# Kernel optimization log

Measured on AMD Instinct MI355X. Metric: run time of the kernel, lower is better.

Reference implementation:

```python
import jax, jax.numpy as jnp
import numpy as np

B, N, E = 2, 2048, 1024
H, D = 16, 64  # num_heads, head_dim
BASE = 10000.0
EPS = 1e-5


def _lrpe(x, offset=0):
    """xmixers Lrpe (lrpe_type=1): activation (silu) then rotary position embedding.
    x: [b, n, h, d] -> [b, n, h, d]"""
    x = jax.nn.silu(x)
    b, n, h, d = x.shape
    inv_freq = BASE ** (-(jnp.arange(d // 2, dtype=jnp.float32) * 2.0) / d)  # [d/2]
    pos = jnp.arange(n, dtype=jnp.float32) + offset
    ang = pos[:, None] * inv_freq[None, :]            # [n, d/2]
    cos = jnp.cos(ang)[None, :, None, :].astype(x.dtype)
    sin = jnp.sin(ang)[None, :, None, :].astype(x.dtype)
    x1, x2 = x[..., : d // 2], x[..., d // 2:]
    return jnp.concatenate([x1 * cos - x2 * sin, x1 * sin + x2 * cos], axis=-1)


def setup_inputs() -> dict:
    key = jax.random.key(0)
    ks = jax.random.split(key, 8)
    std = 0.02
    return {
        "x": jax.random.normal(ks[0], (B, N, E), dtype=jnp.float32),
        "Wq": jax.random.normal(ks[1], (E, E), dtype=jnp.float32) * std,
        "Wk": jax.random.normal(ks[2], (E, E), dtype=jnp.float32) * std,
        "Wv": jax.random.normal(ks[3], (E, E), dtype=jnp.float32) * std,
        "Wo": jax.random.normal(ks[4], (E, E), dtype=jnp.float32) * std,
        "Wg1": jax.random.normal(ks[5], (E, D), dtype=jnp.float32) * std,
        "Wg2": jax.random.normal(ks[6], (D, E), dtype=jnp.float32) * std,
        "gamma": jnp.ones((E,), dtype=jnp.float32),
        "beta": jnp.zeros((E,), dtype=jnp.float32),
    }


def reference(x, Wq, Wk, Wv, Wo, Wg1, Wg2, gamma, beta):
    b, n, e = x.shape
    q = (x @ Wq).reshape(b, n, H, D)
    k = (x @ Wk).reshape(b, n, H, D)
    v = (x @ Wv).reshape(b, n, H, D)

    q = _lrpe(q, offset=0)
    k = _lrpe(k, offset=0)

    # causal linear attention: (q k^T * tril) @ v, no softmax
    energy = jnp.einsum('bnhd,bmhd->bhnm', q, k)            # [b,h,n,n]
    mask = jnp.tril(jnp.ones((n, n), dtype=x.dtype))
    energy = energy * mask
    out = jnp.einsum('bhnm,bmhd->bnhd', energy, v).reshape(b, n, e)

    # output gate: sigmoid(Linear(Linear(x)))
    gate = jax.nn.sigmoid((x @ Wg1) @ Wg2)
    out = out * gate

    # layernorm over embed_dim
    mu = jnp.mean(out, axis=-1, keepdims=True)
    var = jnp.mean(jnp.square(out - mu), axis=-1, keepdims=True)
    out = (out - mu) * jax.lax.rsqrt(var + EPS) * gamma + beta

    return out @ Wo
```

## Files before the change

kernel.cpp:

```cpp
#include <hip/hip_runtime.h>
#include <hip/hip_bf16.h>
#include <math.h>

#define B_ 2
#define N_ 2048
#define E_ 1024
#define H_ 16
#define D_ 64
#define HALF_ 32
#define CK 64
#define NC (N_/CK)
#define BN (B_*N_)
#define TLD 72
#define EPS_ 1e-5f
#define NQKV 3200

using bf16x8  = __attribute__((ext_vector_type(8))) short;
using f32x4   = __attribute__((ext_vector_type(4))) float;
using short4v = __attribute__((ext_vector_type(4))) short;

__device__ __forceinline__ float sigmoid_(float v){ return 1.0f/(1.0f + __expf(-v)); }

__device__ __forceinline__ unsigned short f2bf(float f){
  unsigned u = __float_as_uint(f);
  unsigned r = (u + 0x7fffu + ((u>>16)&1u)) >> 16;
  return (unsigned short)r;
}
__device__ __forceinline__ float bf2f(unsigned short h){
  return __uint_as_float(((unsigned)h)<<16);
}

#define GLDS16(gp, lp) __builtin_amdgcn_global_load_lds( \
    (const __attribute__((address_space(1))) void*)(gp), \
    (__attribute__((address_space(3))) void*)(lp), 16, 0, 0)

__global__ __launch_bounds__(256) void sincos_kernel(float* __restrict__ ct,
                                                     float* __restrict__ st){
  int i = blockIdx.x*256 + threadIdx.x;
  int n = i >> 5, j = i & (HALF_-1);
  double invf = exp(((double)(-2*j)/(double)D_) * log(10000.0));
  double ang = (double)n * invf;
  ct[i] = (float)cos(ang);
  st[i] = (float)sin(ang);
}

__global__ __launch_bounds__(256) void xsplit_kernel(const float* __restrict__ x,
    short* __restrict__ xh, short* __restrict__ xl){
  int i = blockIdx.x*256 + threadIdx.x;
  float4 vv = ((const float4*)x)[i];
  float vs[4] = {vv.x, vv.y, vv.z, vv.w};
  short4v h, l;
  #pragma unroll
  for (int j=0;j<4;j++){
    unsigned short hb = f2bf(vs[j]);
    h[j] = (short)hb;
    l[j] = (short)f2bf(vs[j] - bf2f(hb));
  }
  ((short4v*)xh)[i] = h;
  ((short4v*)xl)[i] = l;
}

__global__ __launch_bounds__(256) void zfill_kernel(short* __restrict__ a,
                                                    short* __restrict__ b){
  int i = blockIdx.x*256 + threadIdx.x;
  short4v z = {0,0,0,0};
  ((short4v*)a)[i] = z;
  ((short4v*)b)[i] = z;
}

__global__ __launch_bounds__(256) void wsplit_kernel(const float* __restrict__ W,
    short* __restrict__ Wth, short* __restrict__ Wtl, int K, int N){
  __shared__ float T[64][65];
  int k0 = blockIdx.x*64, n0 = blockIdx.y*64;
  int tid = threadIdx.x;
  #pragma unroll
  for (int it=0; it<4; ++it){
    int idx = it*256 + tid;
    int r = idx >> 4, c = (idx & 15) << 2;
    float4 v = *(const float4*)&W[(size_t)(k0+r)*N + n0 + c];
    T[c+0][r]=v.x; T[c+1][r]=v.y; T[c+2][r]=v.z; T[c+3][r]=v.w;
  }
  __syncthreads();
  #pragma unroll
  for (int it=0; it<2; ++it){
    int idx = it*256 + tid;
    int r = idx >> 3, c8 = (idx & 7) << 3;
    bf16x8 h, l;
    #pragma unroll
    for (int j=0;j<8;j++){
      float v = T[r][c8+j];
      unsigned short hb = f2bf(v);
      h[j] = (short)hb;
      l[j] = (short)f2bf(v - bf2f(hb));
    }
    size_t o = (size_t)(n0+r)*K + k0 + c8;
    *(bf16x8*)&Wth[o] = h;
    *(bf16x8*)&Wtl[o] = l;
  }
}

template<int EPI>
__global__ __launch_bounds__(256,2) void gemm_mfma(
    const short* __restrict__ Ah, const short* __restrict__ Al,
    const short* __restrict__ Bh, const short* __restrict__ Bl,
    float* __restrict__ C,
    short* __restrict__ Qh, short* __restrict__ Ql,
    short* __restrict__ Kh, short* __restrict__ Kl,
    short* __restrict__ Vh, short* __restrict__ Vl,
    short* __restrict__ G1h, short* __restrict__ G1l,
    const float* __restrict__ ct, const float* __restrict__ st,
    int M, int N, int K)
{
  __shared__ __align__(16) short sAh[128*64];
  __shared__ __align__(16) short sAl[128*64];
  __shared__ __align__(16) short sBh[128*64];
  __shared__ __align__(16) short sBl[128*64];
  const int tid = threadIdx.x;
  const int l = tid & 63, w = tid >> 6;
  const int wm = w >> 1, wn = w & 1;
  const int m0 = blockIdx.x*128, n0 = blockIdx.y*128;
  const int Kb = K*2;
  f32x4 acc[4][4] = {};

  const char* gAh = (const char*)Ah;
  const char* gAl = (const char*)Al;
  const char* gBh = (const char*)Bh;
  const char* gBl = (const char*)Bl;

  const int nkt = K/64;
  for (int kt = 0; kt < nkt; ++kt){
    const int kbyte = kt*128;
    #pragma unroll
    for (int i=0;i<4;i++){
      int p   = i*4096 + tid*16;
      int row = p >> 7;
      int c   = (p & 127) ^ ((row & 7) << 4);
      size_t goA = (size_t)(m0+row)*Kb + kbyte + c;
      size_t goB = (size_t)(n0+row)*Kb + kbyte + c;
      char* lbase = (char*)nullptr;
      (void)lbase;
      GLDS16(gAh + goA, (char*)sAh + i*4096 + w*1024);
      GLDS16(gAl + goA, (char*)sAl + i*4096 + w*1024);
      GLDS16(gBh + goB, (char*)sBh + i*4096 + w*1024);
      GLDS16(gBl + goB, (char*)sBl + i*4096 + w*1024);
    }
    __syncthreads();
    #pragma unroll
    for (int kb=0;kb<2;kb++){
      const int cb = kb*64 + (l>>4)*16;
      bf16x8 ah[4], al[4], bh2[4], bl2[4];
      #pragma unroll
      for (int mb=0;mb<4;mb++){
        int row = wm*64 + mb*16 + (l&15);
        int off = row*128 + (cb ^ ((row&7)<<4));
        ah[mb] = *(const bf16x8*)((const char*)sAh + off);
        al[mb] = *(const bf16x8*)((const char*)sAl + off);
      }
      #pragma unroll
      for (int nb=0;nb<4;nb++){
        int row = wn*64 + nb*16 + (l&15);
        int off = row*128 + (cb ^ ((row&7)<<4));
        bh2[nb] = *(const bf16x8*)((const char*)sBh + off);
        bl2[nb] = *(const bf16x8*)((const char*)sBl + off);
      }
      #pragma unroll
      for (int mb=0;mb<4;mb++)
        #pragma unroll
        for (int nb=0;nb<4;nb++){
          acc[mb][nb] = __builtin_amdgcn_mfma_f32_16x16x32_bf16(ah[mb], bh2[nb], acc[mb][nb], 0,0,0);
          acc[mb][nb] = __builtin_amdgcn_mfma_f32_16x16x32_bf16(ah[mb], bl2[nb], acc[mb][nb], 0,0,0);
          acc[mb][nb] = __builtin_amdgcn_mfma_f32_16x16x32_bf16(al[mb], bh2[nb], acc[mb][nb], 0,0,0);
        }
    }
    __syncthreads();
  }

  if (EPI == 0){
    #pragma unroll
    for (int mb=0;mb<4;mb++)
      #pragma unroll
      for (int nb=0;nb<4;nb++)
        #pragma unroll
        for (int r=0;r<4;r++){
          int row = m0 + wm*64 + mb*16 + (l>>4)*4 + r;
          int colg = n0 + wn*64 + nb*16 + (l&15);
          C[(size_t)row*N + colg] = acc[mb][nb][r];
        }
  } else {
    const int colg0 = n0 + wn*64;
    if (colg0 < 2048){
      short* dh = (colg0 < 1024) ? Qh : Kh;
      short* dl = (colg0 < 1024) ? Ql : Kl;
      const int ebase = colg0 & 1023;
      #pragma unroll
      for (int mb=0;mb<4;mb++)
        #pragma unroll
        for (int nbp=0;nbp<2;nbp++)
          #pragma unroll
          for (int r=0;r<4;r++){
            int row = m0 + wm*64 + mb*16 + (l>>4)*4 + r;
            int d1 = nbp*16 + (l&15);
            float a1 = acc[mb][nbp][r];
            float a2 = acc[mb][nbp+2][r];
            float x1 = a1 * sigmoid_(a1);
            float x2 = a2 * sigmoid_(a2);
            int n = row & (N_-1);
            float cv = ct[n*HALF_ + d1];
            float sv = st[n*HALF_ + d1];
            float r1 = x1*cv - x2*sv;
            float r2 = x1*sv + x2*cv;
            size_t o1 = (size_t)row*E_ + ebase + d1;
            size_t o2 = o1 + HALF_;
            unsigned short h1 = f2bf(r1);
            dh[o1] = (short)h1; dl[o1] = (short)f2bf(r1 - bf2f(h1));
            unsigned short h2 = f2bf(r2);
            dh[o2] = (short)h2; dl[o2] = (short)f2bf(r2 - bf2f(h2));
          }
    } else if (colg0 < 3072){
      #pragma unroll
      for (int mb=0;mb<4;mb++)
        #pragma unroll
        for (int nb=0;nb<4;nb++)
          #pragma unroll
          for (int r=0;r<4;r++){
            int row = m0 + wm*64 + mb*16 + (l>>4)*4 + r;
            int e = colg0 - 2048 + nb*16 + (l&15);
            float v = acc[mb][nb][r];
            unsigned short hb = f2bf(v);
            Vh[(size_t)row*E_ + e] = (short)hb;
            Vl[(size_t)row*E_ + e] = (short)f2bf(v - bf2f(hb));
          }
    } else if (colg0 < 3136){
      #pragma unroll
      for (int mb=0;mb<4;mb++)
        #pragma unroll
        for (int nb=0;nb<4;nb++)
          #pragma unroll
          for (int r=0;r<4;r++){
            int row = m0 + wm*64 + mb*16 + (l>>4)*4 + r;
            int e = nb*16 + (l&15);
            float v = acc[mb][nb][r];
            unsigned short hb = f2bf(v);
            G1h[(size_t)row*D_ + e] = (short)hb;
            G1l[(size_t)row*D_ + e] = (short)f2bf(v - bf2f(hb));
          }
    }
  }
}

__global__ __launch_bounds__(256) void chunk_kv_kernel(
    const short* __restrict__ kh, const short* __restrict__ kl,
    const short* __restrict__ vh, const short* __restrict__ vl,
    float* __restrict__ kvbuf)
{
  __shared__ __align__(16) short sKth[64*TLD], sKtl[64*TLD];
  __shared__ __align__(16) short sVth[64*TLD], sVtl[64*TLD];
  int bid = blockIdx.x;
  int c = bid & (NC-1), bh = bid >> 5;
  int b = bh >> 4, h = bh & 15;
  int tid = threadIdx.x;
  const int l = tid & 63, w = tid >> 6;
  const size_t rb = ((size_t)(b*N_ + c*CK))*E_ + h*D_;
  #pragma unroll
  for (int it=0; it<4; ++it){
    int f = it*256 + tid;
    int m = f >> 4, d0 = (f & 15) << 2;
    short4v a  = *(const short4v*)(kh + rb + (size_t)m*E_ + d0);
    short4v b2 = *(const short4v*)(kl + rb + (size_t)m*E_ + d0);
    short4v cc = *(const short4v*)(vh + rb + (size_t)m*E_ + d0);
    short4v dd = *(const short4v*)(vl + rb + (size_t)m*E_ + d0);
    #pragma unroll
    for (int j=0;j<4;j++){
      sKth[(d0+j)*TLD + m] = a[j];
      sKtl[(d0+j)*TLD + m] = b2[j];
      sVth[(d0+j)*TLD + m] = cc[j];
      sVtl[(d0+j)*TLD + m] = dd[j];
    }
  }
  __syncthreads();
  f32x4 acc[4] = {};
  #pragma unroll
  for (int ks=0; ks<2; ++ks){
    int acb = ks*64 + (l>>4)*16;
    int arow = w*16 + (l&15);
    bf16x8 aH = *(const bf16x8*)((const char*)sKth + arow*(TLD*2) + acb);
    bf16x8 aL = *(const bf16x8*)((const char*)sKtl + arow*(TLD*2) + acb);
    #pragma unroll
    for (int db=0; db<4; ++db){
      int brow = db*16 + (l&15);
      bf16x8 bH = *(const bf16x8*)((const char*)sVth + brow*(TLD*2) + acb);
      bf16x8 bL = *(const bf16x8*)((const char*)sVtl + brow*(TLD*2) + acb);
      acc[db] = __builtin_amdgcn_mfma_f32_16x16x32_bf16(aH, bH, acc[db],0,0,0);
      acc[db] = __builtin_amdgcn_mfma_f32_16x16x32_bf16(aH, bL, acc[db],0,0,0);
      acc[db] = __builtin_amdgcn_mfma_f32_16x16x32_bf16(aL, bH, acc[db],0,0,0);
    }
  }
  float* outp = kvbuf + ((size_t)bh*NC + c)*D_*D_;
  #pragma unroll
  for (int db=0;db<4;db++)
    #pragma unroll
    for (int r=0;r<4;r++){
      int din = w*16 + (l>>4)*4 + r;
      int dout = db*16 + (l&15);
      outp[(size_t)din*D_ + dout] = acc[db][r];
    }
}

__global__ __launch_bounds__(256) void kv_scan_kernel(float* __restrict__ kvbuf){
  int bh = blockIdx.x >> 4, seg = blockIdx.x & 15;
  int e = seg*256 + threadIdx.x;
  float* base = kvbuf + (size_t)bh*NC*D_*D_ + e;
  float run = 0.f;
  #pragma unroll 4
  for (int c=0;c<NC;c++){
    float v = base[(size_t)c*D_*D_];
    base[(size_t)c*D_*D_] = run;
    run += v;
  }
}

__global__ __launch_bounds__(256) void attn_mfma_kernel(
    const short* __restrict__ qh, const short* __restrict__ ql,
    const short* __restrict__ kh, const short* __restrict__ kl,
    const short* __restrict__ vh, const short* __restrict__ vl,
    const float* __restrict__ kvbuf, float* __restrict__ attn)
{
  __shared__ __align__(16) short sQh[4096], sQl[4096];
  __shared__ __align__(16) short sKh[4096], sKl[4096];
  __shared__ __align__(16) short sVth[64*TLD], sVtl[64*TLD];
  __shared__ __align__(16) short sKVth[64*TLD], sKVtl[64*TLD];
  const int tid = threadIdx.x;
  const int l = tid & 63, w = tid >> 6;
  const int bid = blockIdx.x;
  const int c = bid & (NC-1), bh = bid >> 5;
  const int b = bh >> 4, h = bh & 15;
  const size_t rowbase = (size_t)(b*N_ + c*CK);

  #pragma unroll
  for (int p=0;p<2;p++){
    int base = p*4096 + w*1024;
    int db = base + l*16;
    int row = db >> 7, col = db & 127;
    size_t src = ((rowbase + row)*E_ + h*D_)*2 + (size_t)(col ^ ((row&7)<<4));
    GLDS16((const char*)qh + src, (char*)sQh + base);
    GLDS16((const char*)ql + src, (char*)sQl + base);
    GLDS16((const char*)kh + src, (char*)sKh + base);
    GLDS16((const char*)kl + src, (char*)sKl + base);
  }

  {
    const short* vhb = vh + rowbase*E_ + h*D_;
    const short* vlb = vl + rowbase*E_ + h*D_;
    const float* kvb = kvbuf + ((size_t)bh*NC + c)*D_*D_;
    #pragma unroll
    for (int it=0; it<4; ++it){
      int f = it*256 + tid;
      int m = f >> 4, d0 = (f & 15) << 2;
      short4v a  = *(const short4v*)(vhb + (size_t)m*E_ + d0);
      short4v b2 = *(const short4v*)(vlb + (size_t)m*E_ + d0);
      float4 kvv = *(const float4*)(kvb + m*D_ + d0);
      float kvs[4] = {kvv.x,kvv.y,kvv.z,kvv.w};
      #pragma unroll
      for (int j=0;j<4;j++){
        sVth[(d0+j)*TLD + m] = a[j];
        sVtl[(d0+j)*TLD + m] = b2[j];
        unsigned short hb = f2bf(kvs[j]);
        sKVth[(d0+j)*TLD + m] = (short)hb;
        sKVtl[(d0+j)*TLD + m] = (short)f2bf(kvs[j] - bf2f(hb));
      }
    }
  }
  __syncthreads();

  f32x4 sacc[4] = {};
  #pragma unroll
  for (int ks=0; ks<2; ++ks){
    int arow = w*16 + (l&15);
    int acb = ks*64 + (l>>4)*16;
    int aoff = arow*128 + (acb ^ ((arow&7)<<4));
    bf16x8 aH = *(const bf16x8*)((const char*)sQh + aoff);
    bf16x8 aL = *(const bf16x8*)((const char*)sQl + aoff);
    #pragma unroll
    for (int nb=0;nb<4;nb++){
      int brow = nb*16 + (l&15);
      int boff = brow*128 + (acb ^ ((brow&7)<<4));
      bf16x8 bH = *(const bf16x8*)((const char*)sKh + boff);
      bf16x8 bL = *(const bf16x8*)((const char*)sKl + boff);
      sacc[nb] = __builtin_amdgcn_mfma_f32_16x16x32_bf16(aH, bH, sacc[nb],0,0,0);
      sacc[nb] = __builtin_amdgcn_mfma_f32_16x16x32_bf16(aH, bL, sacc[nb],0,0,0);
      sacc[nb] = __builtin_amdgcn_mfma_f32_16x16x32_bf16(aL, bH, sacc[nb],0,0,0);
    }
  }
  __syncthreads();
  #pragma unroll
  for (int nb=0;nb<4;nb++)
    #pragma unroll
    for (int r=0;r<4;r++){
      int n = w*16 + (l>>4)*4 + r;
      int m = nb*16 + (l&15);
      float sv = (m <= n) ? sacc[nb][r] : 0.0f;
      unsigned short hb = f2bf(sv);
      int off = n*128 + ((2*m) ^ ((n&7)<<4));
      *(short*)((char*)sKh + off) = (short)hb;
      *(short*)((char*)sKl + off) = (short)f2bf(sv - bf2f(hb));
    }
  __syncthreads();

  f32x4 oacc[4] = {};
  #pragma unroll
  for (int ks=0; ks<2; ++ks){
    int arow = w*16 + (l&15);
    int acb = ks*64 + (l>>4)*16;
    int aoff = arow*128 + (acb ^ ((arow&7)<<4));
    bf16x8 sH = *(const bf16x8*)((const char*)sKh + aoff);
    bf16x8 sL = *(const bf16x8*)((const char*)sKl + aoff);
    bf16x8 qH = *(const bf16x8*)((const char*)sQh + aoff);
    bf16x8 qL = *(const bf16x8*)((const char*)sQl + aoff);
    #pragma unroll
    for (int db=0; db<4; ++db){
      int brow = db*16 + (l&15);
      bf16x8 vH  = *(const bf16x8*)((const char*)sVth  + brow*(TLD*2) + acb);
      bf16x8 vL  = *(const bf16x8*)((const char*)sVtl  + brow*(TLD*2) + acb);
      bf16x8 kvH = *(const bf16x8*)((const char*)sKVth + brow*(TLD*2) + acb);
      bf16x8 kvL = *(const bf16x8*)((const char*)sKVtl + brow*(TLD*2) + acb);
      oacc[db] = __builtin_amdgcn_mfma_f32_16x16x32_bf16(sH, vH,  oacc[db],0,0,0);
      oacc[db] = __builtin_amdgcn_mfma_f32_16x16x32_bf16(sH, vL,  oacc[db],0,0,0);
      oacc[db] = __builtin_amdgcn_mfma_f32_16x16x32_bf16(sL, vH,  oacc[db],0,0,0);
      oacc[db] = __builtin_amdgcn_mfma_f32_16x16x32_bf16(qH, kvH, oacc[db],0,0,0);
      oacc[db] = __builtin_amdgcn_mfma_f32_16x16x32_bf16(qH, kvL, oacc[db],0,0,0);
      oacc[db] = __builtin_amdgcn_mfma_f32_16x16x32_bf16(qL, kvH, oacc[db],0,0,0);
    }
  }
  float* ob = attn + rowbase*E_ + h*D_;
  #pragma unroll
  for (int db=0;db<4;db++)
    #pragma unroll
    for (int r=0;r<4;r++){
      int n = w*16 + (l>>4)*4 + r;
      int d = db*16 + (l&15);
      ob[(size_t)n*E_ + d] = oacc[db][r];
    }
}

__global__ __launch_bounds__(256) void gate_ln_kernel(const float* __restrict__ attn,
    const float* __restrict__ g2,
    const float* __restrict__ gamma, const float* __restrict__ beta,
    short* __restrict__ yh, short* __restrict__ yl)
{
  __shared__ float red[8];
  __shared__ float stats[2];
  int r = blockIdx.x, tid = threadIdx.x;
  float vals[4]; float s=0.f, sq=0.f;
  #pragma unroll
  for (int i=0;i<4;i++){
    int e = i*256 + tid;
    float a = attn[(size_t)r*E_ + e];
    float g = g2[(size_t)r*E_ + e];
    float val = a * sigmoid_(g);
    vals[i] = val; s += val; sq += val*val;
  }
  #pragma unroll
  for (int off=32; off>=1; off>>=1){
    s  += __shfl_down(s,  off, 64);
    sq += __shfl_down(sq, off, 64);
  }
  int lane = tid & 63, wid = tid >> 6;
  if (lane == 0){ red[wid] = s; red[4+wid] = sq; }
  __syncthreads();
  if (tid == 0){
    float ts = red[0]+red[1]+red[2]+red[3];
    float tq = red[4]+red[5]+red[6]+red[7];
    float mu = ts / (float)E_;
    float var = tq / (float)E_ - mu*mu;
    stats[0] = mu; stats[1] = rsqrtf(var + EPS_);
  }
  __syncthreads();
  float mu = stats[0], rs = stats[1];
  #pragma unroll
  for (int i=0;i<4;i++){
    int e = i*256 + tid;
    float yv = (vals[i]-mu)*rs*gamma[e] + beta[e];
    unsigned short hb = f2bf(yv);
    yh[(size_t)r*E_ + e] = (short)hb;
    yl[(size_t)r*E_ + e] = (short)f2bf(yv - bf2f(hb));
  }
}

extern "C" void kernel_launch(void* const* d_in, const int* in_sizes, int n_in,
                              void* d_out, int out_size, void* d_ws, size_t ws_size,
                              hipStream_t stream) {
  const float* x    = (const float*)d_in[0];
  const float* Wq   = (const float*)d_in[1];
  const float* Wk   = (const float*)d_in[2];
  const float* Wv   = (const float*)d_in[3];
  const float* Wo   = (const float*)d_in[4];
  const float* Wg1  = (const float*)d_in[5];
  const float* Wg2  = (const float*)d_in[6];
  const float* gamma= (const float*)d_in[7];
  const float* beta = (const float*)d_in[8];
  float* out = (float*)d_out;

  char* ws = (char*)d_ws;
  const size_t MB = 1024*1024;
  float* g2    = (float*)(ws + 0*MB);
  float* attnb = (float*)(ws + 16*MB);
  short* xh    = (short*)(ws + 32*MB);
  short* xl    = (short*)(ws + 40*MB);
  short* vh    = (short*)(ws + 48*MB);
  short* vl    = (short*)(ws + 56*MB);
  short* qhb   = (short*)(ws + 64*MB);
  short* qlb   = (short*)(ws + 72*MB);
  short* khb   = (short*)(ws + 80*MB);
  short* klb   = (short*)(ws + 88*MB);
  short* g1h   = (short*)(ws + 96*MB);
  short* g1l   = (short*)(ws + 96*MB + 512*1024);
  float* kv    = (float*)(ws + 96*MB);
  short* wqkvh = (short*)(ws + 112*MB);
  short* wqkvl = (short*)(ws + 119*MB);
  short* woh   = (short*)(ws + 126*MB);
  short* wol   = (short*)(ws + 128*MB);
  short* wg2h  = (short*)(ws + 130*MB);
  short* wg2l  = (short*)(ws + 130*MB + 128*1024);
  float* ct    = (float*)(ws + 130*MB + 256*1024);
  float* st    = (float*)(ws + 130*MB + 512*1024);
  short* yh    = xh;
  short* yl    = xl;

  dim3 blk(256);
  sincos_kernel<<<dim3(N_*HALF_/256), blk, 0, stream>>>(ct, st);
  xsplit_kernel<<<dim3(BN*E_/4/256), blk, 0, stream>>>(x, xh, xl);
  wsplit_kernel<<<dim3(16,16), blk, 0, stream>>>(Wq, wqkvh,             wqkvl,             E_, E_);
  wsplit_kernel<<<dim3(16,16), blk, 0, stream>>>(Wk, wqkvh + 1024*1024, wqkvl + 1024*1024, E_, E_);
  wsplit_kernel<<<dim3(16,16), blk, 0, stream>>>(Wv, wqkvh + 2048*1024, wqkvl + 2048*1024, E_, E_);
  wsplit_kernel<<<dim3(16,1),  blk, 0, stream>>>(Wg1, wqkvh + 3072*1024, wqkvl + 3072*1024, E_, D_);
  zfill_kernel<<<dim3(64), blk, 0, stream>>>(wqkvh + 3136*1024, wqkvl + 3136*1024);
  wsplit_kernel<<<dim3(16,16), blk, 0, stream>>>(Wo, woh, wol, E_, E_);
  wsplit_kernel<<<dim3(1,16),  blk, 0, stream>>>(Wg2, wg2h, wg2l, D_, E_);

  gemm_mfma<3><<<dim3(BN/128, NQKV/128), blk, 0, stream>>>(
      xh, xl, wqkvh, wqkvl, nullptr,
      qhb, qlb, khb, klb, vh, vl, g1h, g1l, ct, st, BN, NQKV, E_);
  gemm_mfma<0><<<dim3(BN/128, E_/128), blk, 0, stream>>>(
      g1h, g1l, wg2h, wg2l, g2,
      nullptr,nullptr,nullptr,nullptr,nullptr,nullptr,nullptr,nullptr,
      nullptr, nullptr, BN, E_, D_);
  chunk_kv_kernel<<<dim3(B_*H_*NC), blk, 0, stream>>>(khb, klb, vh, vl, kv);
  kv_scan_kernel<<<dim3(B_*H_*16), blk, 0, stream>>>(kv);
  attn_mfma_kernel<<<dim3(B_*H_*NC), blk, 0, stream>>>(qhb, qlb, khb, klb, vh, vl, kv, attnb);
  gate_ln_kernel<<<dim3(BN), blk, 0, stream>>>(attnb, g2, gamma, beta, yh, yl);
  gemm_mfma<0><<<dim3(BN/128, E_/128), blk, 0, stream>>>(
      yh, yl, woh, wol, out,
      nullptr,nullptr,nullptr,nullptr,nullptr,nullptr,nullptr,nullptr,
      nullptr, nullptr, BN, E_, E_);
}
```

Baseline: 274.8 us.

## Shrink GEMM tile to 128x64, add block swizzle, drop zero-padding fill

The MFMA GEMM now uses 128x64 output tiles, with each of the four waves owning a 32x64 strip. This halves the B-tile shared memory and accumulator registers, so launch bounds rise to allow three blocks per CU. The grid becomes 1D with an XCD-style swizzle (bid&7 interleave), meant to group neighbouring tiles on the same die for L2 reuse. The fused QKV+G1 GEMM now covers exactly 3136 columns (49 tiles), so the zero-fill kernel for the padded weight rows is removed. More blocks mean more redundant A-tile loads per output and a lower MFMA-to-load ratio per block.

```diff
diff --git a/kernel.cpp b/kernel.cpp
--- a/kernel.cpp
+++ b/kernel.cpp
@@ -60,14 +60,6 @@
   ((short4v*)xl)[i] = l;
 }
 
-__global__ __launch_bounds__(256) void zfill_kernel(short* __restrict__ a,
-                                                    short* __restrict__ b){
-  int i = blockIdx.x*256 + threadIdx.x;
-  short4v z = {0,0,0,0};
-  ((short4v*)a)[i] = z;
-  ((short4v*)b)[i] = z;
-}
-
 __global__ __launch_bounds__(256) void wsplit_kernel(const float* __restrict__ W,
     short* __restrict__ Wth, short* __restrict__ Wtl, int K, int N){
   __shared__ float T[64][65];
@@ -100,7 +92,7 @@
 }
 
 template<int EPI>
-__global__ __launch_bounds__(256,2) void gemm_mfma(
+__global__ __launch_bounds__(256,3) void gemm_mfma(
     const short* __restrict__ Ah, const short* __restrict__ Al,
     const short* __restrict__ Bh, const short* __restrict__ Bl,
     float* __restrict__ C,
@@ -109,18 +101,21 @@
     short* __restrict__ Vh, short* __restrict__ Vl,
     short* __restrict__ G1h, short* __restrict__ G1l,
     const float* __restrict__ ct, const float* __restrict__ st,
-    int M, int N, int K)
+    int M, int N, int K, int nbx)
 {
   __shared__ __align__(16) short sAh[128*64];
   __shared__ __align__(16) short sAl[128*64];
-  __shared__ __align__(16) short sBh[128*64];
-  __shared__ __align__(16) short sBl[128*64];
+  __shared__ __align__(16) short sBh[64*64];
+  __shared__ __align__(16) short sBl[64*64];
   const int tid = threadIdx.x;
   const int l = tid & 63, w = tid >> 6;
-  const int wm = w >> 1, wn = w & 1;
-  const int m0 = blockIdx.x*128, n0 = blockIdx.y*128;
+  const int bid = blockIdx.x;
+  const int cpx = gridDim.x >> 3;
+  const int swz = (bid & 7)*cpx + (bid >> 3);
+  const int bx = swz % nbx, by = swz / nbx;
+  const int m0 = bx*128, n0 = by*64;
   const int Kb = K*2;
-  f32x4 acc[4][4] = {};
+  f32x4 acc[2][4] = {};
 
   const char* gAh = (const char*)Ah;
   const char* gAl = (const char*)Al;
@@ -135,36 +130,40 @@
       int p   = i*4096 + tid*16;
       int row = p >> 7;
       int c   = (p & 127) ^ ((row & 7) << 4);
-      size_t goA = (size_t)(m0+row)*Kb + kbyte + c;
-      size_t goB = (size_t)(n0+row)*Kb + kbyte + c;
-      char* lbase = (char*)nullptr;
-      (void)lbase;
-      GLDS16(gAh + goA, (char*)sAh + i*4096 + w*1024);
-      GLDS16(gAl + goA, (char*)sAl + i*4096 + w*1024);
-      GLDS16(gBh + goB, (char*)sBh + i*4096 + w*1024);
-      GLDS16(gBl + goB, (char*)sBl + i*4096 + w*1024);
+      size_t go = (size_t)(m0+row)*Kb + kbyte + c;
+      GLDS16(gAh + go, (char*)sAh + i*4096 + w*1024);
+      GLDS16(gAl + go, (char*)sAl + i*4096 + w*1024);
+    }
+    #pragma unroll
+    for (int i=0;i<2;i++){
+      int p   = i*4096 + tid*16;
+      int row = p >> 7;
+      int c   = (p & 127) ^ ((row & 7) << 4);
+      size_t go = (size_t)(n0+row)*Kb + kbyte + c;
+      GLDS16(gBh + go, (char*)sBh + i*4096 + w*1024);
+      GLDS16(gBl + go, (char*)sBl + i*4096 + w*1024);
     }
     __syncthreads();
     #pragma unroll
     for (int kb=0;kb<2;kb++){
       const int cb = kb*64 + (l>>4)*16;
-      bf16x8 ah[4], al[4], bh2[4], bl2[4];
-      #pragma unroll
-      for (int mb=0;mb<4;mb++){
-        int row = wm*64 + mb*16 + (l&15);
+      bf16x8 ah[2], al[2], bh2[4], bl2[4];
+      #pragma unroll
+      for (int mb=0;mb<2;mb++){
+        int row = w*32 + mb*16 + (l&15);
         int off = row*128 + (cb ^ ((row&7)<<4));
         ah[mb] = *(const bf16x8*)((const char*)sAh + off);
         al[mb] = *(const bf16x8*)((const char*)sAl + off);
       }
       #pragma unroll
       for (int nb=0;nb<4;nb++){
-        int row = wn*64 + nb*16 + (l&15);
+        int row = nb*16 + (l&15);
         int off = row*128 + (cb ^ ((row&7)<<4));
         bh2[nb] = *(const bf16x8*)((const char*)sBh + off);
         bl2[nb] = *(const bf16x8*)((const char*)sBl + off);
       }
       #pragma unroll
-      for (int mb=0;mb<4;mb++)
+      for (int mb=0;mb<2;mb++)
         #pragma unroll
         for (int nb=0;nb<4;nb++){
           acc[mb][nb] = __builtin_amdgcn_mfma_f32_16x16x32_bf16(ah[mb], bh2[nb], acc[mb][nb], 0,0,0);
@@ -177,28 +176,28 @@
 
   if (EPI == 0){
     #pragma unroll
-    for (int mb=0;mb<4;mb++)
+    for (int mb=0;mb<2;mb++)
       #pragma unroll
       for (int nb=0;nb<4;nb++)
         #pragma unroll
         for (int r=0;r<4;r++){
-          int row = m0 + wm*64 + mb*16 + (l>>4)*4 + r;
-          int colg = n0 + wn*64 + nb*16 + (l&15);
+          int row = m0 + w*32 + mb*16 + (l>>4)*4 + r;
+          int colg = n0 + nb*16 + (l&15);
           C[(size_t)row*N + colg] = acc[mb][nb][r];
         }
   } else {
-    const int colg0 = n0 + wn*64;
+    const int colg0 = n0;
     if (colg0 < 2048){
       short* dh = (colg0 < 1024) ? Qh : Kh;
       short* dl = (colg0 < 1024) ? Ql : Kl;
       const int ebase = colg0 & 1023;
       #pragma unroll
-      for (int mb=0;mb<4;mb++)
+      for (int mb=0;mb<2;mb++)
         #pragma unroll
         for (int nbp=0;nbp<2;nbp++)
           #pragma unroll
           for (int r=0;r<4;r++){
-            int row = m0 + wm*64 + mb*16 + (l>>4)*4 + r;
+            int row = m0 + w*32 + mb*16 + (l>>4)*4 + r;
             int d1 = nbp*16 + (l&15);
             float a1 = acc[mb][nbp][r];
             float a2 = acc[mb][nbp+2][r];
@@ -218,26 +217,26 @@
           }
     } else if (colg0 < 3072){
       #pragma unroll
-      for (int mb=0;mb<4;mb++)
+      for (int mb=0;mb<2;mb++)
         #pragma unroll
         for (int nb=0;nb<4;nb++)
           #pragma unroll
           for (int r=0;r<4;r++){
-            int row = m0 + wm*64 + mb*16 + (l>>4)*4 + r;
+            int row = m0 + w*32 + mb*16 + (l>>4)*4 + r;
             int e = colg0 - 2048 + nb*16 + (l&15);
             float v = acc[mb][nb][r];
             unsigned short hb = f2bf(v);
             Vh[(size_t)row*E_ + e] = (short)hb;
             Vl[(size_t)row*E_ + e] = (short)f2bf(v - bf2f(hb));
           }
-    } else if (colg0 < 3136){
-      #pragma unroll
-      for (int mb=0;mb<4;mb++)
+    } else {
+      #pragma unroll
+      for (int mb=0;mb<2;mb++)
         #pragma unroll
         for (int nb=0;nb<4;nb++)
           #pragma unroll
           for (int r=0;r<4;r++){
-            int row = m0 + wm*64 + mb*16 + (l>>4)*4 + r;
+            int row = m0 + w*32 + mb*16 + (l>>4)*4 + r;
             int e = nb*16 + (l&15);
             float v = acc[mb][nb][r];
             unsigned short hb = f2bf(v);
@@ -533,23 +532,22 @@
   wsplit_kernel<<<dim3(16,16), blk, 0, stream>>>(Wk, wqkvh + 1024*1024, wqkvl + 1024*1024, E_, E_);
   wsplit_kernel<<<dim3(16,16), blk, 0, stream>>>(Wv, wqkvh + 2048*1024, wqkvl + 2048*1024, E_, E_);
   wsplit_kernel<<<dim3(16,1),  blk, 0, stream>>>(Wg1, wqkvh + 3072*1024, wqkvl + 3072*1024, E_, D_);
-  zfill_kernel<<<dim3(64), blk, 0, stream>>>(wqkvh + 3136*1024, wqkvl + 3136*1024);
   wsplit_kernel<<<dim3(16,16), blk, 0, stream>>>(Wo, woh, wol, E_, E_);
   wsplit_kernel<<<dim3(1,16),  blk, 0, stream>>>(Wg2, wg2h, wg2l, D_, E_);
 
-  gemm_mfma<3><<<dim3(BN/128, NQKV/128), blk, 0, stream>>>(
+  gemm_mfma<3><<<dim3(32*49), blk, 0, stream>>>(
       xh, xl, wqkvh, wqkvl, nullptr,
-      qhb, qlb, khb, klb, vh, vl, g1h, g1l, ct, st, BN, NQKV, E_);
-  gemm_mfma<0><<<dim3(BN/128, E_/128), blk, 0, stream>>>(
+      qhb, qlb, khb, klb, vh, vl, g1h, g1l, ct, st, BN, NQKV, E_, 32);
+  gemm_mfma<0><<<dim3(32*16), blk, 0, stream>>>(
       g1h, g1l, wg2h, wg2l, g2,
       nullptr,nullptr,nullptr,nullptr,nullptr,nullptr,nullptr,nullptr,
-      nullptr, nullptr, BN, E_, D_);
+      nullptr, nullptr, BN, E_, D_, 32);
   chunk_kv_kernel<<<dim3(B_*H_*NC), blk, 0, stream>>>(khb, klb, vh, vl, kv);
   kv_scan_kernel<<<dim3(B_*H_*16), blk, 0, stream>>>(kv);
   attn_mfma_kernel<<<dim3(B_*H_*NC), blk, 0, stream>>>(qhb, qlb, khb, klb, vh, vl, kv, attnb);
   gate_ln_kernel<<<dim3(BN), blk, 0, stream>>>(attnb, g2, gamma, beta, yh, yl);
-  gemm_mfma<0><<<dim3(BN/128, E_/128), blk, 0, stream>>>(
+  gemm_mfma<0><<<dim3(32*16), blk, 0, stream>>>(
       yh, yl, woh, wol, out,
       nullptr,nullptr,nullptr,nullptr,nullptr,nullptr,nullptr,nullptr,
-      nullptr, nullptr, BN, E_, E_);
-}
+      nullptr, nullptr, BN, E_, E_, 32);
+}
```

Result: slower. 297.5 us (+8.3%).
